# Performance work log

Hardware: AMD Instinct MI355X
Metric: run time of the kernel (lower is better)

## Reference

```python
import jax, jax.numpy as jnp
import numpy as np
from jax import lax

B, L, D = 2, 1024, 1024
EXPAND, N, K = 2, 16, 4          # expand, d_state, d_conv
DI = EXPAND * D                  # d_inner = 2048
R = (D + 15) // 16               # dt_rank = 64
EPS = 1e-5


def setup_inputs() -> dict:
    key = jax.random.key(0)
    ks = jax.random.split(key, 8)
    x = jax.random.normal(ks[0], (B, L, D), dtype=jnp.float32)
    ln_w = jnp.ones((D,), jnp.float32)
    ln_b = jnp.zeros((D,), jnp.float32)
    W_in = jax.random.normal(ks[1], (D, 2 * DI), jnp.float32) * (1.0 / np.sqrt(D))
    conv_w = jax.random.normal(ks[2], (DI, K), jnp.float32) * 0.2
    conv_b = jnp.zeros((DI,), jnp.float32)
    W_x = jax.random.normal(ks[3], (DI, R + 2 * N), jnp.float32) * (1.0 / np.sqrt(DI))
    W_dt = jax.random.normal(ks[4], (R, DI), jnp.float32) * (1.0 / np.sqrt(R))
    b_dt = jnp.full((DI,), -4.0, jnp.float32)  # softplus(-4) ~ 0.018 dt init
    A_log = jnp.log(jnp.broadcast_to(jnp.arange(1, N + 1, dtype=jnp.float32), (DI, N)))
    D_param = jnp.ones((DI,), jnp.float32)
    W_out = jax.random.normal(ks[5], (DI, D), jnp.float32) * (1.0 / np.sqrt(DI))
    return {"x": x, "ln_w": ln_w, "ln_b": ln_b, "W_in": W_in, "conv_w": conv_w,
            "conv_b": conv_b, "W_x": W_x, "W_dt": W_dt, "b_dt": b_dt,
            "A_log": A_log, "D_param": D_param, "W_out": W_out}


def _mamba_block(x, ln_w, ln_b, W_in, conv_w, conv_b, W_x, W_dt, b_dt, A_log, D_param, W_out):
    # pre-LayerNorm
    mu = jnp.mean(x, axis=-1, keepdims=True)
    xc = x - mu
    var = jnp.mean(xc * xc, axis=-1, keepdims=True)
    h = xc * lax.rsqrt(var + EPS) * ln_w + ln_b          # [B,L,D]

    xz = h @ W_in                                        # [B,L,2*DI]
    xi, z = xz[..., :DI], xz[..., DI:]

    # depthwise causal conv1d, kernel K, left pad K-1
    xp = jnp.pad(xi, ((0, 0), (K - 1, 0), (0, 0)))
    conv = conv_b
    for k in range(K):
        conv = conv + xp[:, k:k + L, :] * conv_w[:, k]
    u = jax.nn.silu(conv)                                # [B,L,DI]

    proj = u @ W_x                                       # [B,L,R+2N]
    dt_r = proj[..., :R]
    Bm = proj[..., R:R + N]                              # [B,L,N]
    Cm = proj[..., R + N:]                               # [B,L,N]
    dt = jax.nn.softplus(dt_r @ W_dt + b_dt)             # [B,L,DI]

    A = -jnp.exp(A_log)                                  # [DI,N]
    dA = jnp.exp(dt[..., None] * A)                      # [B,L,DI,N]
    dBu = (dt * u)[..., None] * Bm[:, :, None, :]        # [B,L,DI,N]

    def comb(e1, e2):
        a1, b1 = e1
        a2, b2 = e2
        return a1 * a2, a2 * b1 + b2

    _, hs = lax.associative_scan(comb, (dA, dBu), axis=1)  # [B,L,DI,N]
    y = jnp.einsum('bldn,bln->bld', hs, Cm) + u * D_param
    y = y * jax.nn.silu(z)
    return x + y @ W_out


def reference(x, ln_w, ln_b, W_in, conv_w, conv_b, W_x, W_dt, b_dt, A_log, D_param, W_out):
    return _mamba_block(x, ln_w, ln_b, W_in, conv_w, conv_b, W_x, W_dt, b_dt,
                        A_log, D_param, W_out)
```

## Files before the change

### kernel.cpp

```cpp
#include <hip/hip_runtime.h>
#include <hip/hip_bf16.h>
#include <math.h>

#define B_ 2
#define L_ 1024
#define D_ 1024
#define DI_ 2048
#define K_ 4
#define N_ 16
#define R_ 64
#define BL_ (B_ * L_)
#define EPS_ 1e-5f

#define IDX4(l) ((l) + (((l) >> 6) << 2))

typedef __attribute__((ext_vector_type(8))) short short8;
typedef __attribute__((ext_vector_type(4))) float f32x4;

__device__ inline unsigned short f2bf(float f) {
    unsigned u = __float_as_uint(f);
    unsigned r = (u + 0x7fffu + ((u >> 16) & 1u)) >> 16;
    return (unsigned short)r;
}
__device__ inline float bf2f(unsigned short s) {
    return __uint_as_float(((unsigned)s) << 16);
}
__device__ inline float fast_silu(float z) {
    return z * __builtin_amdgcn_rcpf(1.f + __expf(-z));
}
#if __has_builtin(__builtin_amdgcn_exp2f)
__device__ inline float fexp2(float x) { return __builtin_amdgcn_exp2f(x); }
#else
__device__ inline float fexp2(float x) { return exp2f(x); }
#endif
__device__ inline void gl_lds16(const void* g, void* l) {
    __builtin_amdgcn_global_load_lds(
        (const __attribute__((address_space(1))) void*)g,
        (__attribute__((address_space(3))) void*)l, 16, 0, 0);
}

template <int CTRL>
__device__ inline float dpp_shr(float x) {
    return __int_as_float(__builtin_amdgcn_update_dpp(
        0, __float_as_int(x), CTRL, 0xf, 0xf, true));
}
__device__ inline float row16_sum(float p) {
    p += dpp_shr<0x111>(p);
    p += dpp_shr<0x112>(p);
    p += dpp_shr<0x114>(p);
    p += dpp_shr<0x118>(p);
    return p;
}

__global__ void ln_kernel(const float* __restrict__ x, const float* __restrict__ w,
                          const float* __restrict__ b, unsigned short* __restrict__ hb) {
    int row = blockIdx.x;
    const float* xr = x + (size_t)row * D_;
    float4 v = ((const float4*)xr)[threadIdx.x];

    __shared__ float red[4];
    float s = v.x + v.y + v.z + v.w;
    for (int off = 1; off < 64; off <<= 1) s += __shfl_xor(s, off, 64);
    if ((threadIdx.x & 63) == 0) red[threadIdx.x >> 6] = s;
    __syncthreads();
    float mu = (red[0] + red[1] + red[2] + red[3]) * (1.0f / D_);
    __syncthreads();
    float cx = v.x - mu, cy = v.y - mu, cz = v.z - mu, cw = v.w - mu;
    float sq = cx*cx + cy*cy + cz*cz + cw*cw;
    for (int off = 1; off < 64; off <<= 1) sq += __shfl_xor(sq, off, 64);
    if ((threadIdx.x & 63) == 0) red[threadIdx.x >> 6] = sq;
    __syncthreads();
    float var = (red[0] + red[1] + red[2] + red[3]) * (1.0f / D_);
    float rstd = rsqrtf(var + EPS_);

    float4 wv = ((const float4*)w)[threadIdx.x];
    float4 bv = ((const float4*)b)[threadIdx.x];
    ushort4 o;
    o.x = f2bf(cx * rstd * wv.x + bv.x);
    o.y = f2bf(cy * rstd * wv.y + bv.y);
    o.z = f2bf(cz * rstd * wv.z + bv.z);
    o.w = f2bf(cw * rstd * wv.w + bv.w);
    ((ushort4*)(hb + (size_t)row * D_))[threadIdx.x] = o;
}

__global__ void transpose_cast_all(const float* __restrict__ W_in, const float* __restrict__ W_x,
                                   const float* __restrict__ W_out,
                                   unsigned short* __restrict__ WinT, unsigned short* __restrict__ WxT,
                                   unsigned short* __restrict__ WoutT) {
    int bid = blockIdx.x;
    const float* W; unsigned short* WT; int K, N, bx, by;
    if (bid < 4096)      { W = W_in;  WT = WinT;  K = 1024; N = 4096; bx = bid & 127; by = bid >> 7; }
    else if (bid < 4288) { int id = bid - 4096; W = W_x;  WT = WxT;  K = DI_; N = 96;   bx = id % 3;  by = id / 3; }
    else                 { int id = bid - 4288; W = W_out; WT = WoutT; K = DI_; N = 1024; bx = id & 31; by = id >> 5; }
    __shared__ float tile[32][33];
    int k0 = by * 32, n0 = bx * 32;
    int tr = threadIdx.x >> 5;
    int tc = threadIdx.x & 31;
#pragma unroll
    for (int i = 0; i < 4; ++i)
        tile[tr + i*8][tc] = W[(size_t)(k0 + tr + i*8) * N + n0 + tc];
    __syncthreads();
#pragma unroll
    for (int i = 0; i < 4; ++i)
        WT[(size_t)(n0 + tr + i*8) * K + k0 + tc] = f2bf(tile[tc][tr + i*8]);
}

template <int BN, int MODE>
__global__ __launch_bounds__(256) void mfma_gemm_bt(
        const unsigned short* __restrict__ A,  int lda,
        const unsigned short* __restrict__ BT, int ldb,
        float* __restrict__ C, int ldc, int Kchunk,
        float* __restrict__ xi, unsigned short* __restrict__ sz) {
    constexpr int NT = BN / 32;
    __shared__ unsigned short As[128 * 32];
    __shared__ unsigned short Bs[BN * 32];

    int tid = threadIdx.x;
    int wave = tid >> 6, lane = tid & 63;
    int lane15 = lane & 15, quad = lane >> 4;
    int wr = wave >> 1, wc = wave & 1;

    int m0 = blockIdx.y * 128;
    int n0 = blockIdx.x * BN;
    int kbeg = blockIdx.z * Kchunk;
    int kend = kbeg + Kchunk;

    f32x4 acc[4][NT];
#pragma unroll
    for (int i = 0; i < 4; ++i)
#pragma unroll
        for (int j = 0; j < NT; ++j) acc[i][j] = (f32x4){0.f, 0.f, 0.f, 0.f};

    constexpr int ACALLS = 8;
    constexpr int BCALLS = BN * 4 / 64;

    for (int k0 = kbeg; k0 < kend; k0 += 32) {
        __syncthreads();
        for (int c = wave; c < ACALLS + BCALLS; c += 4) {
            if (c < ACALLS) {
                int cell = c * 64 + lane;
                int m = cell >> 2, s = cell & 3;
                int q = s ^ (m & 3) ^ ((m >> 2) & 3);
                gl_lds16(A + (size_t)(m0 + m) * lda + k0 + q * 8, &As[c * 512]);
            } else {
                int cell = (c - ACALLS) * 64 + lane;
                int n = cell >> 2, s = cell & 3;
                int q = s ^ (n & 3) ^ ((n >> 2) & 3);
                gl_lds16(BT + (size_t)(n0 + n) * ldb + k0 + q * 8, &Bs[(c - ACALLS) * 512]);
            }
        }
        __syncthreads();

        short8 af[4], bfr[NT];
#pragma unroll
        for (int i = 0; i < 4; ++i) {
            int m = wr * 64 + i * 16 + lane15;
            int s = quad ^ (m & 3) ^ ((m >> 2) & 3);
            af[i] = *(const short8*)&As[m * 32 + s * 8];
        }
#pragma unroll
        for (int j = 0; j < NT; ++j) {
            int n = wc * (NT * 16) + j * 16 + lane15;
            int s = quad ^ (n & 3) ^ ((n >> 2) & 3);
            bfr[j] = *(const short8*)&Bs[n * 32 + s * 8];
        }
#pragma unroll
        for (int i = 0; i < 4; ++i)
#pragma unroll
            for (int j = 0; j < NT; ++j)
                acc[i][j] = __builtin_amdgcn_mfma_f32_16x16x32_bf16(af[i], bfr[j], acc[i][j], 0, 0, 0);
    }

#pragma unroll
    for (int i = 0; i < 4; ++i) {
        int row = m0 + wr * 64 + i * 16 + quad * 4;
#pragma unroll
        for (int j = 0; j < NT; ++j) {
            int col = n0 + wc * (NT * 16) + j * 16 + lane15;
#pragma unroll
            for (int r = 0; r < 4; ++r) {
                float v = acc[i][j][r];
                int rr = row + r;
                if (MODE == 0) {
                    C[(size_t)rr * ldc + col] = v;
                } else if (MODE == 1) {
                    atomicAdd(&C[(size_t)rr * ldc + col], v);
                } else {
                    if (col < DI_) xi[(size_t)rr * DI_ + col] = v;
                    else           sz[(size_t)rr * DI_ + (col - DI_)] = f2bf(fast_silu(v));
                }
            }
        }
    }
}

__global__ void conv_silu_kernel(const float* __restrict__ xi, const float* __restrict__ cw,
                                 const float* __restrict__ cb, unsigned short* __restrict__ ub) {
    int idx = blockIdx.x * blockDim.x + threadIdx.x;
    int c = idx & (DI_ - 1);
    int bl = idx >> 11;
    int l = bl & (L_ - 1);
    float4 w4 = ((const float4*)cw)[c];
    float acc = cb[c];
    const float* base = xi + (size_t)bl * DI_ + c;
    if (l >= 3) {
        acc = fmaf(base[-(size_t)3 * DI_], w4.x, acc);
        acc = fmaf(base[-(size_t)2 * DI_], w4.y, acc);
        acc = fmaf(base[-(size_t)1 * DI_], w4.z, acc);
        acc = fmaf(base[0],                w4.w, acc);
    } else {
        if (l >= 2) acc = fmaf(*(base - 2 * DI_), w4.y, acc);
        if (l >= 1) acc = fmaf(*(base - 1 * DI_), w4.z, acc);
        acc = fmaf(base[0], w4.w, acc);
    }
    ub[idx] = f2bf(fast_silu(acc));
}

__global__ __launch_bounds__(256) void dtprep(
        const float* __restrict__ proj, const float* __restrict__ W_dt,
        const float* __restrict__ b_dt, const unsigned short* __restrict__ ub,
        const unsigned short* __restrict__ szb, const float* __restrict__ Dp,
        float2* __restrict__ dtduT, unsigned int* __restrict__ szdT) {
    __shared__ alignas(16) unsigned char smem[64 * 65 * 8];
    float (*As)[68] = reinterpret_cast<float(*)[68]>(smem);
    float (*Bs)[64] = reinterpret_cast<float(*)[64]>(smem + 4352);
    float2 (*T2)[65] = reinterpret_cast<float2(*)[65]>(smem);
    unsigned int (*TU)[65] = reinterpret_cast<unsigned int(*)[65]>(smem);

    int tid = threadIdx.x;
    int n0 = blockIdx.x * 64;
    int m0 = blockIdx.y * 64;
    int ar = tid >> 2, ak = (tid & 3) << 2;
    int kb = tid >> 4, bc = (tid & 15) << 2;
    int ty = tid >> 4, tx = tid & 15;

    float acc[4][4] = {};
#pragma unroll
    for (int k0 = 0; k0 < R_; k0 += 16) {
        float4 av = *(const float4*)&proj[(size_t)(m0 + ar) * 96 + k0 + ak];
        As[ak + 0][ar] = av.x; As[ak + 1][ar] = av.y;
        As[ak + 2][ar] = av.z; As[ak + 3][ar] = av.w;
        float4 bv = *(const float4*)&W_dt[(size_t)(k0 + kb) * DI_ + n0 + bc];
        Bs[kb][bc + 0] = bv.x; Bs[kb][bc + 1] = bv.y;
        Bs[kb][bc + 2] = bv.z; Bs[kb][bc + 3] = bv.w;
        __syncthreads();
#pragma unroll
        for (int kk = 0; kk < 16; ++kk) {
            float a[4], bb[4];
#pragma unroll
            for (int i = 0; i < 4; ++i) a[i] = As[kk][ty * 4 + i];
#pragma unroll
            for (int j = 0; j < 4; ++j) bb[j] = Bs[kk][tx * 4 + j];
#pragma unroll
            for (int i = 0; i < 4; ++i)
#pragma unroll
                for (int j = 0; j < 4; ++j)
                    acc[i][j] = fmaf(a[i], bb[j], acc[i][j]);
        }
        __syncthreads();
    }

    float4 bd = *(const float4*)&b_dt[n0 + tx * 4];
    float4 dp4 = *(const float4*)&Dp[n0 + tx * 4];
    float bda[4] = {bd.x, bd.y, bd.z, bd.w};
    float dpa[4] = {dp4.x, dp4.y, dp4.z, dp4.w};
    float2 d2[4][4];
    unsigned int su[4][4];
#pragma unroll
    for (int i = 0; i < 4; ++i) {
        int bl = m0 + ty * 4 + i;
        ushort4 u4 = *(const ushort4*)&ub[(size_t)bl * DI_ + n0 + tx * 4];
        ushort4 s4 = *(const ushort4*)&szb[(size_t)bl * DI_ + n0 + tx * 4];
        unsigned short ua[4] = {u4.x, u4.y, u4.z, u4.w};
        unsigned short sa[4] = {s4.x, s4.y, s4.z, s4.w};
#pragma unroll
        for (int j = 0; j < 4; ++j) {
            float v = acc[i][j] + bda[j];
            float dtv = fmaxf(v, 0.f) + __logf(1.f + __expf(-fabsf(v)));
            float uu = bf2f(ua[j]);
            float szv = bf2f(sa[j]);
            d2[i][j] = make_float2(dtv, dtv * uu);
            su[i][j] = ((unsigned)f2bf(uu * dpa[j] * szv) << 16) | (unsigned)f2bf(szv);
        }
    }

#pragma unroll
    for (int i = 0; i < 4; ++i)
#pragma unroll
        for (int j = 0; j < 4; ++j)
            T2[ty * 4 + i][tx * 4 + j] = d2[i][j];
    __syncthreads();
#pragma unroll
    for (int i = 0; i < 8; ++i) {
        int c_l = (tid >> 5) + i * 8;
#pragma unroll
        for (int jj = 0; jj < 2; ++jj) {
            int bl_l = (tid & 31) + jj * 32;
            dtduT[(size_t)(n0 + c_l) * BL_ + m0 + bl_l] = T2[bl_l][c_l];
        }
    }
    __syncthreads();

#pragma unroll
    for (int i = 0; i < 4; ++i)
#pragma unroll
        for (int j = 0; j < 4; ++j)
            TU[ty * 4 + i][tx * 4 + j] = su[i][j];
    __syncthreads();
#pragma unroll
    for (int i = 0; i < 8; ++i) {
        int c_l = (tid >> 5) + i * 8;
#pragma unroll
        for (int jj = 0; jj < 2; ++jj) {
            int bl_l = (tid & 31) + jj * 32;
            szdT[(size_t)(n0 + c_l) * BL_ + m0 + bl_l] = TU[bl_l][c_l];
        }
    }
}

__global__ __launch_bounds__(512, 8) void scan_v8(
        const float2* __restrict__ dtduT, const unsigned int* __restrict__ szdT,
        const float* __restrict__ proj, const float* __restrict__ A_log,
        unsigned short* __restrict__ yzT) {
    int bc = blockIdx.x;
    int b = bc >> 10;
    int cp = bc & 1023;
    int t = threadIdx.x;
    int n = t & 15;
    int cs = (t >> 4) & 1;
    int chunk = t >> 5;
    int c = cp * 2 + cs;

    __shared__ float dd[2][2120];
    __shared__ float sA[16][32];
    __shared__ float sB[16][32];
    __shared__ float ps[2][1096];

    {
        int half = t >> 8;
        int tt = t & 255;
        int l = tt * 4;
        int cload = cp * 2 + half;
        const float4* g = (const float4*)(dtduT + (size_t)cload * BL_ + (size_t)b * L_ + l);
        int il2 = l + ((l >> 6) << 1);
        float* dst = &dd[half][il2 * 2];
        *(float4*)(dst + 0) = g[0];
        *(float4*)(dst + 4) = g[1];
    }
    __syncthreads();

    float A2 = -__expf(A_log[c * N_ + n]) * 1.4426950408889634f;
    int lb = chunk * 64;
    const float* ddp = &dd[cs][(lb + ((lb >> 6) << 1)) * 2];
    const float* pB = proj + (size_t)b * L_ * 96 + R_ + n + (size_t)lb * 96;
    const float* pC = pB + N_;

    float a = 1.f, acc = 0.f;
#pragma unroll
    for (int q = 0; q < 16; ++q) {
        float4 d0 = *(const float4*)(ddp + q * 8);
        float4 d1 = *(const float4*)(ddp + q * 8 + 4);
        float b0 = pB[(q*4 + 0) * 96];
        float b1 = pB[(q*4 + 1) * 96];
        float b2 = pB[(q*4 + 2) * 96];
        float b3 = pB[(q*4 + 3) * 96];
        float e;
        e = fexp2(d0.x * A2); a *= e; acc = fmaf(e, acc, d0.y * b0);
        e = fexp2(d0.z * A2); a *= e; acc = fmaf(e, acc, d0.w * b1);
        e = fexp2(d1.x * A2); a *= e; acc = fmaf(e, acc, d1.y * b2);
        e = fexp2(d1.z * A2); a *= e; acc = fmaf(e, acc, d1.w * b3);
    }
    sA[chunk][cs * 16 + n] = a;
    sB[chunk][cs * 16 + n] = acc;
    __syncthreads();

    if (t < 32) {
        float hc = 0.f;
#pragma unroll
        for (int j = 0; j < 16; ++j) {
            float aj = sA[j][t];
            float bj = sB[j][t];
            sB[j][t] = hc;
            hc = fmaf(aj, hc, bj);
        }
    }
    __syncthreads();
    float h = sB[chunk][cs * 16 + n];

    float* psb = &ps[cs][IDX4(lb)];
#pragma unroll
    for (int q = 0; q < 16; ++q) {
        float4 d0 = *(const float4*)(ddp + q * 8);
        float4 d1 = *(const float4*)(ddp + q * 8 + 4);
        float b0 = pB[(q*4 + 0) * 96], c0 = pC[(q*4 + 0) * 96];
        float b1 = pB[(q*4 + 1) * 96], c1 = pC[(q*4 + 1) * 96];
        float b2 = pB[(q*4 + 2) * 96], c2 = pC[(q*4 + 2) * 96];
        float b3 = pB[(q*4 + 3) * 96], c3 = pC[(q*4 + 3) * 96];
        float e, p0, p1, p2, p3;
        e = fexp2(d0.x * A2); h = fmaf(e, h, d0.y * b0); p0 = row16_sum(h * c0);
        e = fexp2(d0.z * A2); h = fmaf(e, h, d0.w * b1); p1 = row16_sum(h * c1);
        e = fexp2(d1.x * A2); h = fmaf(e, h, d1.y * b2); p2 = row16_sum(h * c2);
        e = fexp2(d1.z * A2); h = fmaf(e, h, d1.w * b3); p3 = row16_sum(h * c3);
        if (n == 15) *(float4*)&psb[q * 4] = (float4){p0, p1, p2, p3};
    }
    __syncthreads();

    {
        int half = t >> 8;
        int tt = t & 255;
        int l = tt * 4;
        int c_out = cp * 2 + half;
        size_t tb = (size_t)c_out * BL_ + (size_t)b * L_;
        const float* pp = &ps[half][IDX4(l)];
        float4 p4 = *(const float4*)pp;
        uint4 sd4 = *(const uint4*)(szdT + tb + l);
        ushort4 o;
        o.x = f2bf(p4.x * bf2f((unsigned short)(sd4.x & 0xffff)) + bf2f((unsigned short)(sd4.x >> 16)));
        o.y = f2bf(p4.y * bf2f((unsigned short)(sd4.y & 0xffff)) + bf2f((unsigned short)(sd4.y >> 16)));
        o.z = f2bf(p4.z * bf2f((unsigned short)(sd4.z & 0xffff)) + bf2f((unsigned short)(sd4.z >> 16)));
        o.w = f2bf(p4.w * bf2f((unsigned short)(sd4.w & 0xffff)) + bf2f((unsigned short)(sd4.w >> 16)));
        *(ushort4*)(yzT + tb + l) = o;
    }
}

__global__ void transpose_y(const unsigned short* __restrict__ yzT, unsigned short* __restrict__ yz) {
    __shared__ unsigned short t[32][33];
    int c0 = blockIdx.y * 32, bl0 = blockIdx.x * 32;
    int r = threadIdx.x >> 5;
    int col = threadIdx.x & 31;
#pragma unroll
    for (int i = 0; i < 4; ++i)
        t[r + i*8][col] = yzT[(size_t)(c0 + r + i*8) * BL_ + bl0 + col];
    __syncthreads();
#pragma unroll
    for (int i = 0; i < 4; ++i)
        yz[(size_t)(bl0 + r + i*8) * DI_ + c0 + col] = t[col][r + i*8];
}

extern "C" void kernel_launch(void* const* d_in, const int* in_sizes, int n_in,
                              void* d_out, int out_size, void* d_ws, size_t ws_size,
                              hipStream_t stream) {
    const float* x       = (const float*)d_in[0];
    const float* ln_w    = (const float*)d_in[1];
    const float* ln_b    = (const float*)d_in[2];
    const float* W_in    = (const float*)d_in[3];
    const float* conv_w  = (const float*)d_in[4];
    const float* conv_b  = (const float*)d_in[5];
    const float* W_x     = (const float*)d_in[6];
    const float* W_dt    = (const float*)d_in[7];
    const float* b_dt    = (const float*)d_in[8];
    const float* A_log   = (const float*)d_in[9];
    const float* D_param = (const float*)d_in[10];
    const float* W_out   = (const float*)d_in[11];
    float* out = (float*)d_out;

    uint8_t* p = (uint8_t*)d_ws;
    unsigned short* hb    = (unsigned short*)p;  p += (size_t)BL_ * D_ * 2;
    unsigned short* WinT  = (unsigned short*)p;  p += (size_t)4096 * 1024 * 2;
    float*          xib   = (float*)p;           p += (size_t)BL_ * DI_ * 4;
    unsigned short* szb   = (unsigned short*)p;  p += (size_t)BL_ * DI_ * 2;
    unsigned short* ub    = (unsigned short*)p;  p += (size_t)BL_ * DI_ * 2;
    unsigned short* WxT   = (unsigned short*)p;  p += (size_t)96 * DI_ * 2;
    float*          proj  = (float*)p;           p += (size_t)BL_ * 96 * 4;
    unsigned short* WoutT = (unsigned short*)p;  p += (size_t)1024 * DI_ * 2;
    float2*         dtduT = (float2*)p;          p += (size_t)BL_ * DI_ * 8;
    unsigned int*   szdT  = (unsigned int*)p;    p += (size_t)BL_ * DI_ * 4;
    unsigned short* yzT   = (unsigned short*)p;  p += (size_t)BL_ * DI_ * 2;
    unsigned short* yzb   = (unsigned short*)d_ws;

    hipMemsetAsync(proj, 0, (size_t)BL_ * 96 * 4, stream);
    hipMemcpyAsync(out, x, (size_t)BL_ * D_ * 4, hipMemcpyDeviceToDevice, stream);

    transpose_cast_all<<<6336, 256, 0, stream>>>(W_in, W_x, W_out, WinT, WxT, WoutT);

    ln_kernel<<<BL_, 256, 0, stream>>>(x, ln_w, ln_b, hb);

    mfma_gemm_bt<128, 3><<<dim3(4096 / 128, BL_ / 128, 1), 256, 0, stream>>>(
        hb, 1024, WinT, 1024, nullptr, 0, 1024, xib, szb);

    conv_silu_kernel<<<(BL_ * DI_) / 256, 256, 0, stream>>>(xib, conv_w, conv_b, ub);

    mfma_gemm_bt<96, 1><<<dim3(1, BL_ / 128, 16), 256, 0, stream>>>(
        ub, DI_, WxT, DI_, proj, 96, 128, nullptr, nullptr);

    dtprep<<<dim3(DI_ / 64, BL_ / 64), 256, 0, stream>>>(
        proj, W_dt, b_dt, ub, szb, D_param, dtduT, szdT);

    scan_v8<<<B_ * DI_ / 2, 512, 0, stream>>>(dtduT, szdT, proj, A_log, yzT);

    transpose_y<<<dim3(BL_ / 32, DI_ / 32), 256, 0, stream>>>(yzT, yzb);

    mfma_gemm_bt<128, 1><<<dim3(1024 / 128, BL_ / 128, 2), 256, 0, stream>>>(
        yzb, DI_, WoutT, DI_, out, 1024, 1024, nullptr, nullptr);
}
```

Measured before the change: 281.1 us.

## Pack B/C into compact buffer, use prefix-sum decay in scan pass 1, swizzle GEMM blocks

The dtprep kernel now copies the B and C columns of proj into a dense 32-float-per-row buffer, so the scan reads 128-byte rows instead of striding across 384-byte proj rows. Scan pass 1 walks each chunk backwards with a running sum of dt, computing exp2(S*A) per step. This removes the serial product chain but keeps one exp per step. The GEMM kernel also remaps block indices in groups of eight to improve L2 locality. The packed buffer sits at a fixed 8 MB offset inside the workspace, inside the region hb/yzb occupies, and relies on yzb not being written until after the scan.

```diff
diff --git a/kernel.cpp b/kernel.cpp
--- a/kernel.cpp
+++ b/kernel.cpp
@@ -120,8 +120,15 @@
     int lane15 = lane & 15, quad = lane >> 4;
     int wr = wave >> 1, wc = wave & 1;
 
-    int m0 = blockIdx.y * 128;
-    int n0 = blockIdx.x * BN;
+    int nxy = gridDim.x * gridDim.y;
+    int flat = blockIdx.y * gridDim.x + blockIdx.x;
+    int cpx = nxy >> 3;
+    int swz = (flat & 7) * cpx + (flat >> 3);
+    int bx = swz % gridDim.x;
+    int by = swz / gridDim.x;
+
+    int m0 = by * 128;
+    int n0 = bx * BN;
     int kbeg = blockIdx.z * Kchunk;
     int kend = kbeg + Kchunk;
 
@@ -220,7 +227,8 @@
         const float* __restrict__ proj, const float* __restrict__ W_dt,
         const float* __restrict__ b_dt, const unsigned short* __restrict__ ub,
         const unsigned short* __restrict__ szb, const float* __restrict__ Dp,
-        float2* __restrict__ dtduT, unsigned int* __restrict__ szdT) {
+        float2* __restrict__ dtduT, unsigned int* __restrict__ szdT,
+        float* __restrict__ bcpack) {
     __shared__ alignas(16) unsigned char smem[64 * 65 * 8];
     float (*As)[68] = reinterpret_cast<float(*)[68]>(smem);
     float (*Bs)[64] = reinterpret_cast<float(*)[64]>(smem + 4352);
@@ -233,6 +241,17 @@
     int ar = tid >> 2, ak = (tid & 3) << 2;
     int kb = tid >> 4, bc = (tid & 15) << 2;
     int ty = tid >> 4, tx = tid & 15;
+
+    if (blockIdx.x == 0) {
+#pragma unroll
+        for (int r = 0; r < 2; ++r) {
+            int idx = tid * 2 + r;
+            int row = idx >> 3;
+            int c4  = idx & 7;
+            float4 v = *(const float4*)&proj[(size_t)(m0 + row) * 96 + 64 + c4 * 4];
+            *(float4*)&bcpack[(size_t)(m0 + row) * 32 + c4 * 4] = v;
+        }
+    }
 
     float acc[4][4] = {};
 #pragma unroll
@@ -318,9 +337,9 @@
     }
 }
 
-__global__ __launch_bounds__(512, 8) void scan_v8(
+__global__ __launch_bounds__(512, 8) void scan_v9(
         const float2* __restrict__ dtduT, const unsigned int* __restrict__ szdT,
-        const float* __restrict__ proj, const float* __restrict__ A_log,
+        const float* __restrict__ bcpack, const float* __restrict__ A_log,
         unsigned short* __restrict__ yzT) {
     int bc = blockIdx.x;
     int b = bc >> 10;
@@ -352,24 +371,30 @@
     float A2 = -__expf(A_log[c * N_ + n]) * 1.4426950408889634f;
     int lb = chunk * 64;
     const float* ddp = &dd[cs][(lb + ((lb >> 6) << 1)) * 2];
-    const float* pB = proj + (size_t)b * L_ * 96 + R_ + n + (size_t)lb * 96;
-    const float* pC = pB + N_;
-
-    float a = 1.f, acc = 0.f;
-#pragma unroll
-    for (int q = 0; q < 16; ++q) {
-        float4 d0 = *(const float4*)(ddp + q * 8);
-        float4 d1 = *(const float4*)(ddp + q * 8 + 4);
-        float b0 = pB[(q*4 + 0) * 96];
-        float b1 = pB[(q*4 + 1) * 96];
-        float b2 = pB[(q*4 + 2) * 96];
-        float b3 = pB[(q*4 + 3) * 96];
-        float e;
-        e = fexp2(d0.x * A2); a *= e; acc = fmaf(e, acc, d0.y * b0);
-        e = fexp2(d0.z * A2); a *= e; acc = fmaf(e, acc, d0.w * b1);
-        e = fexp2(d1.x * A2); a *= e; acc = fmaf(e, acc, d1.y * b2);
-        e = fexp2(d1.z * A2); a *= e; acc = fmaf(e, acc, d1.w * b3);
-    }
+    const float* pb0 = bcpack + ((size_t)b * L_ + lb) * 32 + n;
+    const float* pb1 = pb0 + 32 * 32;
+
+    float S = 0.f, acc = 0.f;
+#pragma unroll
+    for (int h2 = 1; h2 >= 0; --h2) {
+        const float* pb = h2 ? pb1 : pb0;
+        const float* dph = ddp + h2 * 64;
+#pragma unroll
+        for (int q = 7; q >= 0; --q) {
+            float4 d0 = *(const float4*)(dph + q * 8);
+            float4 d1 = *(const float4*)(dph + q * 8 + 4);
+            float b3 = pb[(q*4 + 3) * 32];
+            float b2 = pb[(q*4 + 2) * 32];
+            float b1v = pb[(q*4 + 1) * 32];
+            float b0 = pb[(q*4 + 0) * 32];
+            float e;
+            e = fexp2(S * A2); acc = fmaf(e, d1.w * b3, acc); S += d1.z;
+            e = fexp2(S * A2); acc = fmaf(e, d1.y * b2, acc); S += d1.x;
+            e = fexp2(S * A2); acc = fmaf(e, d0.w * b1v, acc); S += d0.z;
+            e = fexp2(S * A2); acc = fmaf(e, d0.y * b0, acc); S += d0.x;
+        }
+    }
+    float a = fexp2(S * A2);
     sA[chunk][cs * 16 + n] = a;
     sB[chunk][cs * 16 + n] = acc;
     __syncthreads();
@@ -389,19 +414,25 @@
 
     float* psb = &ps[cs][IDX4(lb)];
 #pragma unroll
-    for (int q = 0; q < 16; ++q) {
-        float4 d0 = *(const float4*)(ddp + q * 8);
-        float4 d1 = *(const float4*)(ddp + q * 8 + 4);
-        float b0 = pB[(q*4 + 0) * 96], c0 = pC[(q*4 + 0) * 96];
-        float b1 = pB[(q*4 + 1) * 96], c1 = pC[(q*4 + 1) * 96];
-        float b2 = pB[(q*4 + 2) * 96], c2 = pC[(q*4 + 2) * 96];
-        float b3 = pB[(q*4 + 3) * 96], c3 = pC[(q*4 + 3) * 96];
-        float e, p0, p1, p2, p3;
-        e = fexp2(d0.x * A2); h = fmaf(e, h, d0.y * b0); p0 = row16_sum(h * c0);
-        e = fexp2(d0.z * A2); h = fmaf(e, h, d0.w * b1); p1 = row16_sum(h * c1);
-        e = fexp2(d1.x * A2); h = fmaf(e, h, d1.y * b2); p2 = row16_sum(h * c2);
-        e = fexp2(d1.z * A2); h = fmaf(e, h, d1.w * b3); p3 = row16_sum(h * c3);
-        if (n == 15) *(float4*)&psb[q * 4] = (float4){p0, p1, p2, p3};
+    for (int h2 = 0; h2 < 2; ++h2) {
+        const float* pb = h2 ? pb1 : pb0;
+        const float* dph = ddp + h2 * 64;
+        float* psh = psb + h2 * 32;
+#pragma unroll
+        for (int q = 0; q < 8; ++q) {
+            float4 d0 = *(const float4*)(dph + q * 8);
+            float4 d1 = *(const float4*)(dph + q * 8 + 4);
+            float b0 = pb[(q*4 + 0) * 32], c0 = pb[(q*4 + 0) * 32 + 16];
+            float b1v = pb[(q*4 + 1) * 32], c1 = pb[(q*4 + 1) * 32 + 16];
+            float b2 = pb[(q*4 + 2) * 32], c2 = pb[(q*4 + 2) * 32 + 16];
+            float b3 = pb[(q*4 + 3) * 32], c3 = pb[(q*4 + 3) * 32 + 16];
+            float e, p0, p1, p2, p3;
+            e = fexp2(d0.x * A2); h = fmaf(e, h, d0.y * b0); p0 = row16_sum(h * c0);
+            e = fexp2(d0.z * A2); h = fmaf(e, h, d0.w * b1v); p1 = row16_sum(h * c1);
+            e = fexp2(d1.x * A2); h = fmaf(e, h, d1.y * b2); p2 = row16_sum(h * c2);
+            e = fexp2(d1.z * A2); h = fmaf(e, h, d1.w * b3); p3 = row16_sum(h * c3);
+            if (n == 15) *(float4*)&psh[q * 4] = (float4){p0, p1, p2, p3};
+        }
     }
     __syncthreads();
 
@@ -467,6 +498,7 @@
     unsigned int*   szdT  = (unsigned int*)p;    p += (size_t)BL_ * DI_ * 4;
     unsigned short* yzT   = (unsigned short*)p;  p += (size_t)BL_ * DI_ * 2;
     unsigned short* yzb   = (unsigned short*)d_ws;
+    float*          bcpack = (float*)((uint8_t*)d_ws + (size_t)8 * 1024 * 1024);
 
     hipMemsetAsync(proj, 0, (size_t)BL_ * 96 * 4, stream);
     hipMemcpyAsync(out, x, (size_t)BL_ * D_ * 4, hipMemcpyDeviceToDevice, stream);
@@ -484,9 +516,9 @@
         ub, DI_, WxT, DI_, proj, 96, 128, nullptr, nullptr);
 
     dtprep<<<dim3(DI_ / 64, BL_ / 64), 256, 0, stream>>>(
-        proj, W_dt, b_dt, ub, szb, D_param, dtduT, szdT);
-
-    scan_v8<<<B_ * DI_ / 2, 512, 0, stream>>>(dtduT, szdT, proj, A_log, yzT);
+        proj, W_dt, b_dt, ub, szb, D_param, dtduT, szdT, bcpack);
+
+    scan_v9<<<B_ * DI_ / 2, 512, 0, stream>>>(dtduT, szdT, bcpack, A_log, yzT);
 
     transpose_y<<<dim3(BL_ / 32, DI_ / 32), 256, 0, stream>>>(yzT, yzb);
 
```

Result: no change. 283.0 us (+0.7%).
